# Optimization experiments

Measured on AMD Instinct MI355X. Metric: run time of the kernel, lower is better.

The kernel has to match this reference:

```python
import jax, jax.numpy as jnp
import numpy as np

CUTOFF = 14      # Fock cutoff per qumode
M = 3            # qumodes per circuit
N_CIRCUITS = 2
N_LAYERS = 2
BATCH = 1024
TWO_PI = 6.283185307179586

# ---- mode operators (Strawberry Fields convention, hbar=2 -> X = a + a^dagger) ----
A = jnp.diag(jnp.sqrt(jnp.arange(1, CUTOFF, dtype=jnp.float32)), 1).astype(jnp.complex64)  # annihilation
AD = A.conj().T
NVEC = jnp.arange(CUTOFF)
XOP = A + AD
A1 = jnp.kron(AD, A)   # a^dag (x) b
A2 = jnp.kron(A, AD)   # a (x) b^dag


def _expm(H, s=12, terms=14):
    """Fixed scaling-and-squaring matrix exponential (differentiable, jit-safe)."""
    B = H * (2.0 ** -s)
    n = H.shape[-1]
    out = jnp.eye(n, dtype=H.dtype)
    term = jnp.eye(n, dtype=H.dtype)
    for kk in range(1, terms + 1):
        term = term @ (B / float(kk))
        out = out + term
    for _ in range(s):
        out = out @ out
    return out


def disp_gate(mag, phi):
    alpha = (mag * jnp.exp(1j * phi)).astype(jnp.complex64)
    return _expm(alpha * AD - jnp.conj(alpha) * A)


def squeeze_gate(rr, phi):
    z = (rr * jnp.exp(1j * phi)).astype(jnp.complex64)
    return _expm(0.5 * (jnp.conj(z) * (A @ A) - z * (AD @ AD)))


def rot_gate(phi):
    return jnp.diag(jnp.exp(1j * phi * NVEC)).astype(jnp.complex64)


def kerr_gate(kap):
    return jnp.diag(jnp.exp(1j * kap * (NVEC ** 2))).astype(jnp.complex64)


def bs_gate(theta, phi):
    H = theta.astype(jnp.complex64) * (jnp.exp(1j * phi) * A1 - jnp.exp(-1j * phi) * A2)
    return _expm(H).reshape(CUTOFF, CUTOFF, CUTOFF, CUTOFF)


# PennyLane rectangular-mesh interferometer pair ordering
def bs_pairs(m):
    return [(i, i + 1) for l in range(m) for i in range(m - 1) if (l + i) % 2 != 1]

PAIRS = bs_pairs(M)  # K = M(M-1)/2 pairs


def apply1(U, psi, m):
    return jnp.moveaxis(jnp.tensordot(U, psi, axes=([1], [m])), 0, m)


def apply2(U4, psi, m):
    return jnp.moveaxis(jnp.tensordot(U4, psi, axes=([2, 3], [m, m + 1])), (0, 1), (m, m + 1))


def circuit_outputs(x_c, th1, ph1, vph1, rr, phr, th2, ph2, vph2, aa, pha, kk):
    # precompute all weight-dependent gates once (shared across the batch)
    gates = []
    for l in range(N_LAYERS):
        for p, (m1, _) in enumerate(PAIRS):
            gates.append((bs_gate(th1[l, p], ph1[l, p]), m1, True))
        for m_ in range(M):
            gates.append((rot_gate(vph1[l, m_]), m_, False))
        for m_ in range(M):
            gates.append((squeeze_gate(rr[l, m_], phr[l, m_]), m_, False))
        for p, (m1, _) in enumerate(PAIRS):
            gates.append((bs_gate(th2[l, p], ph2[l, p]), m1, True))
        for m_ in range(M):
            gates.append((rot_gate(vph2[l, m_]), m_, False))
        for m_ in range(M):
            gates.append((disp_gate(aa[l, m_], pha[l, m_]), m_, False))
        for m_ in range(M):
            gates.append((kerr_gate(kk[l, m_]), m_, False))
    vac = jnp.zeros((CUTOFF,) * M, jnp.complex64).at[(0,) * M].set(1.0)

    def run_one(xs):
        psi = vac
        # DisplacementEmbedding: D(x_i, 0) on wire i
        for m_ in range(M):
            psi = apply1(disp_gate(xs[m_], jnp.float32(0.0)), psi, m_)
        for U, m_, two in gates:
            psi = apply2(U, psi, m_) if two else apply1(U, psi, m_)
        return jnp.stack([jnp.real(jnp.vdot(psi, apply1(XOP, psi, m_))) for m_ in range(M)])

    return jax.vmap(run_one)(x_c)


def setup_inputs() -> dict:
    key = jax.random.key(0)
    ks = jax.random.split(key, 12)
    u = lambda kk, shape, hi: jax.random.uniform(kk, shape, jnp.float32, 0.0, hi)
    Kp = M * (M - 1) // 2
    sh_k = (N_CIRCUITS, N_LAYERS, Kp)
    sh_m = (N_CIRCUITS, N_LAYERS, M)
    return {
        'x': u(ks[0], (BATCH, N_CIRCUITS * M), 1.0),
        'theta_1': u(ks[1], sh_k, TWO_PI), 'phi_1': u(ks[2], sh_k, TWO_PI),
        'varphi_1': u(ks[3], sh_m, TWO_PI),
        'r': u(ks[4], sh_m, 0.1), 'phi_r': u(ks[5], sh_m, TWO_PI),
        'theta_2': u(ks[6], sh_k, TWO_PI), 'phi_2': u(ks[7], sh_k, TWO_PI),
        'varphi_2': u(ks[8], sh_m, TWO_PI),
        'a': u(ks[9], sh_m, 0.1), 'phi_a': u(ks[10], sh_m, TWO_PI),
        'k': u(ks[11], sh_m, TWO_PI),
    }


def reference(x, theta_1, phi_1, varphi_1, r, phi_r, theta_2, phi_2, varphi_2, a, phi_a, k):
    outs = []
    for ci in range(N_CIRCUITS):
        x_c = x[:, ci * M:(ci + 1) * M]
        outs.append(circuit_outputs(x_c, theta_1[ci], phi_1[ci], varphi_1[ci],
                                     r[ci], phi_r[ci], theta_2[ci], phi_2[ci],
                                     varphi_2[ci], a[ci], phi_a[ci], k[ci]))
    return jnp.concatenate(outs, axis=1)  # (BATCH, n_outputs)
```

## Files before the change

### kernel.cpp

```cpp
#include <hip/hip_runtime.h>
#include <hip/hip_bf16.h>

typedef __hip_bfloat16 bf16;

#define CUT 14
#define D2 196
#define D3 2744
#define GSTRIDE 3584

#define SX 0
#define STH1 1
#define SPH1 2
#define SVPH1 3
#define SR 4
#define SPHR 5
#define STH2 6
#define SPH2 7
#define SVPH2 8
#define SA 9
#define SPHA 10
#define SK 11

__constant__ unsigned char c_PN[256] = {
13,13,13,13,13,13,13,13,13,13,13,13,13,13,
12,12,12,12,12,12,12,12,12,12,12,12,12,
14,14,14,14,14,14,14,14,14,14,14,14,14,
11,11,11,11,11,11,11,11,11,11,11,11,
15,15,15,15,15,15,15,15,15,15,15,15,
10,10,10,10,10,10,10,10,10,10,10,
16,16,16,16,16,16,16,16,16,16,16,
9,9,9,9,9,9,9,9,9,9,
17,17,17,17,17,17,17,17,17,17,
8,8,8,8,8,8,8,8,8,
18,18,18,18,18,18,18,18,18,
3,3,3,3,
7,7,7,7,7,7,7,7,
19,19,19,19,19,19,19,19,
6,6,6,6,6,6,6,
20,20,20,20,20,20,20,
5,5,5,5,5,5,
21,21,21,21,21,21,
4,4,4,4,4,
22,22,22,22,22,
23,23,23,23,
2,2,2,
24,24,24,
1,1,
25,25,
0,
26,
255,255,255,255,255,255,255,255,255,255,255,255,255,255,255,
255,255,255,255,255,255,255,255,255,255,255,255,255,255,255,
255,255,255,255,255,255,255,255,255,255,255,255,255,255,255,
255,255,255,255,255,255,255,255,255,255,255,255,255,255,255};
__constant__ unsigned char c_PA[256] = {
0,1,2,3,4,5,6,7,8,9,10,11,12,13,
0,1,2,3,4,5,6,7,8,9,10,11,12,
1,2,3,4,5,6,7,8,9,10,11,12,13,
0,1,2,3,4,5,6,7,8,9,10,11,
2,3,4,5,6,7,8,9,10,11,12,13,
0,1,2,3,4,5,6,7,8,9,10,
3,4,5,6,7,8,9,10,11,12,13,
0,1,2,3,4,5,6,7,8,9,
4,5,6,7,8,9,10,11,12,13,
0,1,2,3,4,5,6,7,8,
5,6,7,8,9,10,11,12,13,
0,1,2,3,
0,1,2,3,4,5,6,7,
6,7,8,9,10,11,12,13,
0,1,2,3,4,5,6,
7,8,9,10,11,12,13,
0,1,2,3,4,5,
8,9,10,11,12,13,
0,1,2,3,4,
9,10,11,12,13,
10,11,12,13,
0,1,2,
11,12,13,
0,1,
12,13,
0,
13,
0,0,0,0,0,0,0,0,0,0,0,0,0,0,0,
0,0,0,0,0,0,0,0,0,0,0,0,0,0,0,
0,0,0,0,0,0,0,0,0,0,0,0,0,0,0,
0,0,0,0,0,0,0,0,0,0,0,0,0,0,0};
__constant__ short c_PSTART[27] = {194,190,184,124,170,158,144,128,106,86,64,40,14,0,
                                   27,52,75,96,115,136,151,164,175,180,187,192,195};

struct P12 { const void* p[12]; };

__device__ float2 g_gp[24 * GSTRIDE];
__device__ float2 g_gsr[12 * D2];
__device__ float2 g_grdk[12 * D2];
__device__ int    g_flag;
__device__ int    g_map[12];

__device__ __forceinline__ float2 cfma2(float2 acc, float2 a, float2 b) {
    acc.x = fmaf(a.x, b.x, fmaf(-a.y, b.y, acc.x));
    acc.y = fmaf(a.x, b.y, fmaf(a.y, b.x, acc.y));
    return acc;
}
__device__ __forceinline__ float2 cmul2(float2 a, float2 b) {
    return make_float2(a.x*b.x - a.y*b.y, a.x*b.y + a.y*b.x);
}
__device__ __forceinline__ float load_raw(const void* p, int i, int f32) {
    return f32 ? ((const float*)p)[i]
               : __bfloat162float(((const bf16*)p)[i]);
}

__device__ void detect_layout(const P12& P, int ix, int* sh)
{
    int t = threadIdx.x;
    if (t < 13) sh[13 + t] = 0;
    __syncthreads();
    const unsigned int* u = (const unsigned int*)P.p[ix];
    if (t < 256) {
        if (u[t] & 0x8000u) atomicOr(&sh[25], 1);
    }
    __syncthreads();
    int f = sh[25] != 0 ? 1 : 0;
    if (t < 144) {
        int p = t / 12, j = t - (t/12)*12;
        if (p != ix) {
            float v = fabsf(load_raw(P.p[p], j, f));
            atomicMax(&sh[13 + p], __float_as_int(v));
        }
    }
    __syncthreads();
    if (t == 0) {
        int mask = 0;
        for (int i = 0; i < 12; ++i) {
            if (i == ix) continue;
            if (__int_as_float(sh[13 + i]) < 0.2f) mask |= (1 << i);
        }
        const int dict_map[12]  = {0,1,2,3,4,5,6,7,8,9,10,11};
        const int alpha_map[12] = {11,7,2,9,6,5,8,3,10,0,4,1};
        const int* m = (ix == 11 && mask == ((1<<0)|(1<<6))) ? alpha_map : dict_map;
        for (int i = 0; i < 12; ++i) sh[i] = m[i];
        sh[12] = f;
    }
    __syncthreads();
}

__device__ void expm_lds(float2* B, float2* TERM, float2* OUT, float2* TMP, int s, int t)
{
    const int s2 = s * s;
    if (t < s2) { B[t].x *= (1.0f/1024.0f); B[t].y *= (1.0f/1024.0f); }
    __syncthreads();
    if (t < s2) {
        float2 id = make_float2((t % (s + 1) == 0) ? 1.0f : 0.0f, 0.0f);
        TERM[t] = id; OUT[t] = id;
    }
    __syncthreads();
    for (int kk = 1; kk <= 10; ++kk) {
        if (t < s2) {
            int i = t / s, j = t - i * s;
            float2 acc = make_float2(0.f, 0.f);
            for (int k = 0; k < s; ++k) acc = cfma2(acc, TERM[i*s+k], B[k*s+j]);
            float inv = 1.0f / (float)kk;
            TMP[t] = make_float2(acc.x*inv, acc.y*inv);
        }
        __syncthreads();
        if (t < s2) { TERM[t] = TMP[t]; OUT[t].x += TMP[t].x; OUT[t].y += TMP[t].y; }
        __syncthreads();
    }
    for (int q = 0; q < 10; ++q) {
        if (t < s2) {
            int i = t / s, j = t - i * s;
            float2 acc = make_float2(0.f, 0.f);
            for (int k = 0; k < s; ++k) acc = cfma2(acc, OUT[i*s+k], OUT[k*s+j]);
            TMP[t] = acc;
        }
        __syncthreads();
        if (t < s2) OUT[t] = TMP[t];
        __syncthreads();
    }
}

__global__ __launch_bounds__(256)
void build_all(P12 P, int ix)
{
    __shared__ float2 B[D2], TERM[D2], OUT[D2], TMP[D2];
    __shared__ int sh[26];
    int t = threadIdx.x;
    detect_layout(P, ix, sh);
    const int f32 = sh[12];
    if (blockIdx.x == 0 && t == 0) {
        for (int i = 0; i < 12; ++i) g_map[i] = sh[i];
        g_flag = f32;
    }
    #define LS(slot, i) load_raw(P.p[sh[(slot)]], (i), f32)

    if (blockIdx.x < 648) {
        int gate = blockIdx.x / 27;
        int n    = blockIdx.x % 27;
        int cc   = gate / 12;
        int l    = (gate / 6) % 2;
        int slot = gate % 6;
        int p    = slot % 3;
        int pidx = (cc*2 + l)*3 + p;
        float th = LS(slot < 3 ? STH1 : STH2, pidx);
        float ph = LS(slot < 3 ? SPH1 : SPH2, pidx);
        float cph, sph; sincosf(ph, &sph, &cph);
        int cmin = max(0, n - 13);
        int cmax = min(13, n);
        int s = cmax - cmin + 1;
        if (t < s*s) {
            int i = t / s, j = t - (t/s)*s;
            float2 h = make_float2(0.f, 0.f);
            int cj = cmin + j;
            if (i == j + 1) {
                float sq = th * sqrtf((float)((cj+1)*(n-cj)));
                h = make_float2(sq*cph, sq*sph);
            } else if (i == j - 1) {
                float sq = th * sqrtf((float)(cj*(n-cj+1)));
                h = make_float2(-sq*cph, sq*sph);
            }
            B[t] = h;
        }
        __syncthreads();
        expm_lds(B, TERM, OUT, TMP, s, t);
        if (t < s*14) {
            int ii = t / 14, ci = t - (t/14)*14;
            float2 v = (ci < s) ? OUT[ii*s + ci] : make_float2(0.f, 0.f);
            g_gp[gate*GSTRIDE + ci*256 + (c_PSTART[n] + ii)] = v;
        }
    } else {
        int q = blockIdx.x - 648;
        int pidx = q >> 1;
        int half = q & 1;
        if (half == 0) {
            float rv = LS(SR, pidx);
            float pv = LS(SPHR, pidx);
            float cp, sp; sincosf(pv, &sp, &cp);
            if (t < D2) {
                int i = t / 14, j = t - (t/14)*14;
                float2 h = make_float2(0.f, 0.f);
                if (j == i + 2) {
                    float s = 0.5f * rv * sqrtf((float)((i+1)*(i+2)));
                    h = make_float2(s*cp, -s*sp);
                } else if (i == j + 2) {
                    float s = 0.5f * rv * sqrtf((float)((j+1)*(j+2)));
                    h = make_float2(-s*cp, -s*sp);
                }
                B[t] = h;
            }
            __syncthreads();
            expm_lds(B, TERM, OUT, TMP, 14, t);
            float v1 = LS(SVPH1, pidx);
            if (t < D2) {
                int j = t - (t/14)*14;
                float cs, sn; sincosf(v1 * (float)j, &sn, &cs);
                g_gsr[pidx*D2 + t] = cmul2(OUT[t], make_float2(cs, sn));
            }
        } else {
            float av = LS(SA, pidx);
            float pav = LS(SPHA, pidx);
            float ca, sa; sincosf(pav, &sa, &ca);
            if (t < D2) {
                int i = t / 14, j = t - (t/14)*14;
                float2 h = make_float2(0.f, 0.f);
                if (i == j + 1) {
                    float s = av * sqrtf((float)(j+1));
                    h = make_float2(s*ca, s*sa);
                } else if (j == i + 1) {
                    float s = av * sqrtf((float)(i+1));
                    h = make_float2(-s*ca, s*sa);
                }
                B[t] = h;
            }
            __syncthreads();
            expm_lds(B, TERM, OUT, TMP, 14, t);
            float v2 = LS(SVPH2, pidx);
            float kv = LS(SK, pidx);
            if (t < D2) {
                int i = t / 14, j = t - (t/14)*14;
                float ang = kv * (float)(i*i) + v2 * (float)j;
                float cs, sn; sincosf(ang, &sn, &cs);
                g_grdk[pidx*D2 + t] = cmul2(OUT[t], make_float2(cs, sn));
            }
        }
    }
    #undef LS
}


template<int PAIR>
__device__ void apply_bs(const float2* __restrict__ G, float2* ps, int t,
                         int aP, int bP, int nP, int sP, int cminP)
{
    if (nP != 255) {
        float2 u[14];
        #pragma unroll
        for (int ci = 0; ci < 14; ++ci) u[ci] = G[ci*256 + t];
        float2 acc[14];
        #pragma unroll
        for (int k = 0; k < 14; ++k) acc[k] = make_float2(0.f, 0.f);
        #pragma unroll
        for (int ci = 0; ci < 14; ++ci) {
            if (ci < sP) {
                int c = cminP + ci;
                int d = nP - c;
                const float2* sp = (PAIR == 0) ? (ps + (c*14 + d)*14) : (ps + c*14 + d);
                #pragma unroll
                for (int k = 0; k < 14; ++k)
                    acc[k] = cfma2(acc[k], u[ci], sp[PAIR == 0 ? k : k*196]);
            }
        }
        float2* dp = (PAIR == 0) ? (ps + (aP*14 + bP)*14) : (ps + aP*14 + bP);
        #pragma unroll
        for (int k = 0; k < 14; ++k) dp[PAIR == 0 ? k : k*196] = acc[k];
    }
    __syncthreads();
}

template<int MODE>
__device__ void apply_single(const float2* __restrict__ U, float2* ps, int t)
{
    if (t < D2) {
        int base, stride;
        if (MODE == 0)      { base = t; stride = 196; }
        else if (MODE == 1) { base = (t/14)*196 + (t % 14); stride = 14; }
        else                { base = t*14; stride = 1; }
        float2 fib[14];
        #pragma unroll
        for (int j = 0; j < 14; ++j) fib[j] = ps[base + j*stride];
        #pragma unroll
        for (int i = 0; i < 14; ++i) {
            float2 acc = make_float2(0.f, 0.f);
            #pragma unroll
            for (int j = 0; j < 14; ++j) acc = cfma2(acc, U[i*14 + j], fib[j]);
            ps[base + i*stride] = acc;
        }
    }
    __syncthreads();
}

#define ABS0(G) apply_bs<0>(G, ps, t, aP, bP, nP, sP, cminP);
#define ABS1(G) apply_bs<1>(G, ps, t, aP, bP, nP, sP, cminP);

__global__ __launch_bounds__(256)
void qcircuit(P12 P, float* __restrict__ out)
{
    __shared__ float2 ps[D3];
    __shared__ float cohr[3][14];
    __shared__ float red[12];
    int t = threadIdx.x;
    int b = blockIdx.x >> 1;
    int c = blockIdx.x & 1;
    int base6 = b*6 + c*3;
    int f32 = g_flag;

    int nP = (int)c_PN[t];
    int aP = (int)c_PA[t];
    int bP = (nP != 255) ? (nP - aP) : 0;
    int cminP = max(0, nP - 13);
    int sP = min(13, nP) - cminP + 1;

    if (t < 42) {
        int m = t / 14, n = t - (t/14)*14;
        float xv = load_raw(P.p[g_map[SX]], base6 + m, f32);
        float p = 1.0f;
        for (int q = 0; q < n; ++q) p *= xv;
        float f = 1.0f;
        for (int q = 2; q <= n; ++q) f *= (float)q;
        cohr[m][n] = expf(-0.5f*xv*xv) * p / sqrtf(f);
    }
    __syncthreads();
    for (int idx = t; idx < D3; idx += 256) {
        int i2 = idx % 14, i1 = (idx/14) % 14, i0 = idx / 196;
        ps[idx] = make_float2(cohr[0][i0]*cohr[1][i1]*cohr[2][i2], 0.f);
    }
    __syncthreads();

    for (int l = 0; l < 2; ++l) {
        int gi = c*2 + l;
        const float2* bsb = g_gp + gi*6*GSTRIDE;
        ABS0(bsb + 0*GSTRIDE)
        ABS1(bsb + 1*GSTRIDE)
        ABS0(bsb + 2*GSTRIDE)
        apply_single<0>(g_gsr + (gi*3+0)*D2, ps, t);
        apply_single<1>(g_gsr + (gi*3+1)*D2, ps, t);
        apply_single<2>(g_gsr + (gi*3+2)*D2, ps, t);
        ABS0(bsb + 3*GSTRIDE)
        ABS1(bsb + 4*GSTRIDE)
        ABS0(bsb + 5*GSTRIDE)
        apply_single<0>(g_grdk + (gi*3+0)*D2, ps, t);
        apply_single<1>(g_grdk + (gi*3+1)*D2, ps, t);
        apply_single<2>(g_grdk + (gi*3+2)*D2, ps, t);
    }

    float p0 = 0.f, p1 = 0.f, p2 = 0.f;
    for (int idx = t; idx < D3; idx += 256) {
        int i2 = idx % 14, i1 = (idx/14) % 14, i0 = idx / 196;
        float2 v = ps[idx];
        if (i0 < 13) { float2 w = ps[idx + 196]; p0 += sqrtf((float)(i0+1)) * (v.x*w.x + v.y*w.y); }
        if (i1 < 13) { float2 w = ps[idx + 14];  p1 += sqrtf((float)(i1+1)) * (v.x*w.x + v.y*w.y); }
        if (i2 < 13) { float2 w = ps[idx + 1];   p2 += sqrtf((float)(i2+1)) * (v.x*w.x + v.y*w.y); }
    }
    #pragma unroll
    for (int off = 32; off > 0; off >>= 1) {
        p0 += __shfl_down(p0, off, 64);
        p1 += __shfl_down(p1, off, 64);
        p2 += __shfl_down(p2, off, 64);
    }
    int lane = t & 63, w = t >> 6;
    if (lane == 0) { red[w*3+0] = p0; red[w*3+1] = p1; red[w*3+2] = p2; }
    __syncthreads();
    if (t == 0) {
        float o0 = 0.f, o1 = 0.f, o2 = 0.f;
        for (int q = 0; q < 4; ++q) { o0 += red[q*3]; o1 += red[q*3+1]; o2 += red[q*3+2]; }
        out[base6 + 0] = 2.0f * o0;
        out[base6 + 1] = 2.0f * o1;
        out[base6 + 2] = 2.0f * o2;
    }
}

extern "C" void kernel_launch(void* const* d_in, const int* in_sizes, int n_in,
                              void* d_out, int out_size, void* d_ws, size_t ws_size,
                              hipStream_t stream) {
    (void)d_ws; (void)ws_size;
    P12 P;
    for (int i = 0; i < 12; ++i) P.p[i] = (i < n_in) ? d_in[i] : nullptr;
    float* out = (float*)d_out;

    int ix = 0; long best = -1;
    for (int i = 0; i < 12 && i < n_in; ++i)
        if ((long)in_sizes[i] > best) { best = in_sizes[i]; ix = i; }
    int B = out_size / 6; if (B < 1) B = 1;

    build_all<<<672, 256, 0, stream>>>(P, ix);
    qcircuit<<<2*B, 256, 0, stream>>>(P, out);
}
```

Baseline: 442.7 us.

## Repartition beamsplitter work over all output elements using precomputed index map

The beamsplitter application changes from one thread per (a,b) pair that computes 14 outputs, with threads past 196 sitting idle, to each thread handling about 11 of the 2744 output elements. A per-element index map is built once in an extra build block, and the gate blocks are re-laid out with a new offset table. The aim is to use all 256 threads and cut per-thread register pressure. In exchange it adds index-map loads, a variable-length inner loop, and an extra barrier before writeback, and the function is marked noinline.

```diff
diff --git a/kernel.cpp b/kernel.cpp
--- a/kernel.cpp
+++ b/kernel.cpp
@@ -6,7 +6,6 @@
 #define CUT 14
 #define D2 196
 #define D3 2744
-#define GSTRIDE 3584
 
 #define SX 0
 #define STH1 1
@@ -21,80 +20,17 @@
 #define SPHA 10
 #define SK 11
 
-__constant__ unsigned char c_PN[256] = {
-13,13,13,13,13,13,13,13,13,13,13,13,13,13,
-12,12,12,12,12,12,12,12,12,12,12,12,12,
-14,14,14,14,14,14,14,14,14,14,14,14,14,
-11,11,11,11,11,11,11,11,11,11,11,11,
-15,15,15,15,15,15,15,15,15,15,15,15,
-10,10,10,10,10,10,10,10,10,10,10,
-16,16,16,16,16,16,16,16,16,16,16,
-9,9,9,9,9,9,9,9,9,9,
-17,17,17,17,17,17,17,17,17,17,
-8,8,8,8,8,8,8,8,8,
-18,18,18,18,18,18,18,18,18,
-3,3,3,3,
-7,7,7,7,7,7,7,7,
-19,19,19,19,19,19,19,19,
-6,6,6,6,6,6,6,
-20,20,20,20,20,20,20,
-5,5,5,5,5,5,
-21,21,21,21,21,21,
-4,4,4,4,4,
-22,22,22,22,22,
-23,23,23,23,
-2,2,2,
-24,24,24,
-1,1,
-25,25,
-0,
-26,
-255,255,255,255,255,255,255,255,255,255,255,255,255,255,255,
-255,255,255,255,255,255,255,255,255,255,255,255,255,255,255,
-255,255,255,255,255,255,255,255,255,255,255,255,255,255,255,
-255,255,255,255,255,255,255,255,255,255,255,255,255,255,255};
-__constant__ unsigned char c_PA[256] = {
-0,1,2,3,4,5,6,7,8,9,10,11,12,13,
-0,1,2,3,4,5,6,7,8,9,10,11,12,
-1,2,3,4,5,6,7,8,9,10,11,12,13,
-0,1,2,3,4,5,6,7,8,9,10,11,
-2,3,4,5,6,7,8,9,10,11,12,13,
-0,1,2,3,4,5,6,7,8,9,10,
-3,4,5,6,7,8,9,10,11,12,13,
-0,1,2,3,4,5,6,7,8,9,
-4,5,6,7,8,9,10,11,12,13,
-0,1,2,3,4,5,6,7,8,
-5,6,7,8,9,10,11,12,13,
-0,1,2,3,
-0,1,2,3,4,5,6,7,
-6,7,8,9,10,11,12,13,
-0,1,2,3,4,5,6,
-7,8,9,10,11,12,13,
-0,1,2,3,4,5,
-8,9,10,11,12,13,
-0,1,2,3,4,
-9,10,11,12,13,
-10,11,12,13,
-0,1,2,
-11,12,13,
-0,1,
-12,13,
-0,
-13,
-0,0,0,0,0,0,0,0,0,0,0,0,0,0,0,
-0,0,0,0,0,0,0,0,0,0,0,0,0,0,0,
-0,0,0,0,0,0,0,0,0,0,0,0,0,0,0,
-0,0,0,0,0,0,0,0,0,0,0,0,0,0,0};
-__constant__ short c_PSTART[27] = {194,190,184,124,170,158,144,128,106,86,64,40,14,0,
-                                   27,52,75,96,115,136,151,164,175,180,187,192,195};
+__constant__ int c_SOFF[27] = {0,1,3,6,10,15,21,28,36,45,55,66,78,91,
+                               105,118,130,141,151,160,168,175,181,186,190,193,195};
 
 struct P12 { const void* p[12]; };
 
-__device__ float2 g_gp[24 * GSTRIDE];
+__device__ float2 g_gpad[24 * D3];
 __device__ float2 g_gsr[12 * D2];
 __device__ float2 g_grdk[12 * D2];
-__device__ int    g_flag;
-__device__ int    g_map[12];
+__device__ unsigned int g_emap[D3];
+__device__ int g_flag;
+__device__ int g_map[12];
 
 __device__ __forceinline__ float2 cfma2(float2 acc, float2 a, float2 b) {
     acc.x = fmaf(a.x, b.x, fmaf(-a.y, b.y, acc.x));
@@ -224,13 +160,12 @@
         if (t < s*14) {
             int ii = t / 14, ci = t - (t/14)*14;
             float2 v = (ci < s) ? OUT[ii*s + ci] : make_float2(0.f, 0.f);
-            g_gp[gate*GSTRIDE + ci*256 + (c_PSTART[n] + ii)] = v;
-        }
-    } else {
+            g_gpad[gate*D3 + ci*196 + (c_SOFF[n] + ii)] = v;
+        }
+    } else if (blockIdx.x < 672) {
         int q = blockIdx.x - 648;
         int pidx = q >> 1;
-        int half = q & 1;
-        if (half == 0) {
+        if ((q & 1) == 0) {
             float rv = LS(SR, pidx);
             float pv = LS(SPHR, pidx);
             float cp, sp; sincosf(pv, &sp, &cp);
@@ -281,36 +216,71 @@
                 g_grdk[pidx*D2 + t] = cmul2(OUT[t], make_float2(cs, sn));
             }
         }
+    } else {
+        for (int e = t; e < D3; e += 256) {
+            int cum = 0, n = 13, s = 14, off = 0;
+            for (int q = 0; q < 27; ++q) {
+                int nn = (q == 0) ? 13 : ((q & 1) ? 13 - (q+1)/2 : 13 + q/2);
+                int cmn = max(0, nn-13), cmx = min(13, nn);
+                int ss = cmx - cmn + 1;
+                int sz = 14 * ss;
+                if (e >= cum && e < cum + sz) { n = nn; s = ss; off = e - cum; }
+                cum += sz;
+            }
+            int cmin = max(0, n-13);
+            int k = off / s;
+            int a = cmin + (off - k*s);
+            int spos = c_SOFF[n] + (a - cmin);
+            g_emap[e] = (unsigned)n | ((unsigned)a << 8) |
+                        ((unsigned)k << 16) | ((unsigned)spos << 24);
+        }
     }
     #undef LS
 }
 
-
 template<int PAIR>
-__device__ void apply_bs(const float2* __restrict__ G, float2* ps, int t,
-                         int aP, int bP, int nP, int sP, int cminP)
-{
-    if (nP != 255) {
-        float2 u[14];
-        #pragma unroll
-        for (int ci = 0; ci < 14; ++ci) u[ci] = G[ci*256 + t];
-        float2 acc[14];
-        #pragma unroll
-        for (int k = 0; k < 14; ++k) acc[k] = make_float2(0.f, 0.f);
-        #pragma unroll
-        for (int ci = 0; ci < 14; ++ci) {
-            if (ci < sP) {
-                int c = cminP + ci;
-                int d = nP - c;
-                const float2* sp = (PAIR == 0) ? (ps + (c*14 + d)*14) : (ps + c*14 + d);
-                #pragma unroll
-                for (int k = 0; k < 14; ++k)
-                    acc[k] = cfma2(acc[k], u[ci], sp[PAIR == 0 ? k : k*196]);
-            }
-        }
-        float2* dp = (PAIR == 0) ? (ps + (aP*14 + bP)*14) : (ps + aP*14 + bP);
-        #pragma unroll
-        for (int k = 0; k < 14; ++k) dp[PAIR == 0 ? k : k*196] = acc[k];
+__device__ __attribute__((noinline))
+void apply_bs(const float2* __restrict__ G, float2* ps, int t)
+{
+    float2 acc[11];
+    unsigned int mp[11];
+    #pragma unroll
+    for (int p = 0; p < 11; ++p) {
+        int e = p*256 + t;
+        mp[p] = (e < D3) ? g_emap[e] : 0xFFFFFFFFu;
+    }
+    #pragma unroll
+    for (int p = 0; p < 11; ++p) {
+        acc[p] = make_float2(0.f, 0.f);
+        unsigned int m = mp[p];
+        if (m != 0xFFFFFFFFu) {
+            int n    = m & 0xFF;
+            int k    = (m >> 16) & 0xFF;
+            int spos = (m >> 24) & 0xFF;
+            int cmin = max(0, n-13);
+            int s = min(13, n) - cmin + 1;
+            const float2* gp = G + spos;
+            int src = (PAIR == 0) ? (cmin*14 + (n-cmin))*14 + k
+                                  : k*196 + cmin*14 + (n-cmin);
+            const int dsrc = (PAIR == 0) ? 182 : 13;
+            for (int ci = 0; ci < s; ++ci) {
+                acc[p] = cfma2(acc[p], gp[ci*196], ps[src]);
+                src += dsrc;
+            }
+        }
+    }
+    __syncthreads();
+    #pragma unroll
+    for (int p = 0; p < 11; ++p) {
+        unsigned int m = mp[p];
+        if (m != 0xFFFFFFFFu) {
+            int n = m & 0xFF;
+            int a = (m >> 8) & 0xFF;
+            int k = (m >> 16) & 0xFF;
+            int dst = (PAIR == 0) ? (a*14 + (n-a))*14 + k
+                                  : k*196 + a*14 + (n-a);
+            ps[dst] = acc[p];
+        }
     }
     __syncthreads();
 }
@@ -337,9 +307,6 @@
     __syncthreads();
 }
 
-#define ABS0(G) apply_bs<0>(G, ps, t, aP, bP, nP, sP, cminP);
-#define ABS1(G) apply_bs<1>(G, ps, t, aP, bP, nP, sP, cminP);
-
 __global__ __launch_bounds__(256)
 void qcircuit(P12 P, float* __restrict__ out)
 {
@@ -352,12 +319,6 @@
     int base6 = b*6 + c*3;
     int f32 = g_flag;
 
-    int nP = (int)c_PN[t];
-    int aP = (int)c_PA[t];
-    int bP = (nP != 255) ? (nP - aP) : 0;
-    int cminP = max(0, nP - 13);
-    int sP = min(13, nP) - cminP + 1;
-
     if (t < 42) {
         int m = t / 14, n = t - (t/14)*14;
         float xv = load_raw(P.p[g_map[SX]], base6 + m, f32);
@@ -376,16 +337,16 @@
 
     for (int l = 0; l < 2; ++l) {
         int gi = c*2 + l;
-        const float2* bsb = g_gp + gi*6*GSTRIDE;
-        ABS0(bsb + 0*GSTRIDE)
-        ABS1(bsb + 1*GSTRIDE)
-        ABS0(bsb + 2*GSTRIDE)
+        const float2* bsb = g_gpad + gi*6*D3;
+        apply_bs<0>(bsb + 0*D3, ps, t);
+        apply_bs<1>(bsb + 1*D3, ps, t);
+        apply_bs<0>(bsb + 2*D3, ps, t);
         apply_single<0>(g_gsr + (gi*3+0)*D2, ps, t);
         apply_single<1>(g_gsr + (gi*3+1)*D2, ps, t);
         apply_single<2>(g_gsr + (gi*3+2)*D2, ps, t);
-        ABS0(bsb + 3*GSTRIDE)
-        ABS1(bsb + 4*GSTRIDE)
-        ABS0(bsb + 5*GSTRIDE)
+        apply_bs<0>(bsb + 3*D3, ps, t);
+        apply_bs<1>(bsb + 4*D3, ps, t);
+        apply_bs<0>(bsb + 5*D3, ps, t);
         apply_single<0>(g_grdk + (gi*3+0)*D2, ps, t);
         apply_single<1>(g_grdk + (gi*3+1)*D2, ps, t);
         apply_single<2>(g_grdk + (gi*3+2)*D2, ps, t);
@@ -430,6 +391,6 @@
         if ((long)in_sizes[i] > best) { best = in_sizes[i]; ix = i; }
     int B = out_size / 6; if (B < 1) B = 1;
 
-    build_all<<<672, 256, 0, stream>>>(P, ix);
+    build_all<<<673, 256, 0, stream>>>(P, ix);
     qcircuit<<<2*B, 256, 0, stream>>>(P, out);
 }
```

Result: slower. 744.7 us (+68.2%).
